# Optimization experiments

Measured on AMD Instinct MI355X. Metric: run time of the kernel, lower is better.

The kernel has to match this reference:

```python
import jax, jax.numpy as jnp
import numpy as np

B, H, KVH, D = 32, 32, 8, 128          # batch, q heads, kv heads, head_size
S = 2048                                # context length per sequence
BLOCK_SIZE = 16                         # tokens per cache block
NUM_BLOCKS = B * (S // BLOCK_SIZE)      # 4096
BASE = 10000.0
SCALE = 1.0 / D ** 0.5


def setup_inputs() -> dict:
    key = jax.random.key(0)
    kq, kk, kv = jax.random.split(key, 3)
    query = jax.random.normal(kq, (B, H, D), dtype=jnp.float32)
    # paged KV cache: [num_blocks, block_size * kv_heads * head_size]
    k_cache = jax.random.normal(kk, (NUM_BLOCKS, BLOCK_SIZE * KVH * D), dtype=jnp.float32)
    v_cache = jax.random.normal(kv, (NUM_BLOCKS, BLOCK_SIZE * KVH * D), dtype=jnp.float32)
    # contiguous slot layout: slot[i, p] = i * S + p  (>=0 means valid)
    slot_mapping = jnp.arange(B * S, dtype=jnp.int32).reshape(B, S)
    # per-sequence token positions 0..S-1
    positions = jnp.broadcast_to(jnp.arange(S, dtype=jnp.int32), (B, S))
    return {"query": query, "k_cache": k_cache, "v_cache": v_cache,
            "slot_mapping": slot_mapping, "positions": positions}


def _rope(x, pos):
    """x: [B, h, s, D], pos: [B, s] int -> rotary-embedded x (RotaryEmbedding.forward)."""
    inv_freq = 1.0 / (BASE ** (jnp.arange(0, D, 2, dtype=jnp.float32) / D))   # [D/2]
    freqs = pos[..., None].astype(jnp.float32) * inv_freq                     # [B, s, D/2]
    emb = jnp.concatenate([freqs, freqs], axis=-1)                            # [B, s, D]
    cos = jnp.cos(emb)[:, None]                                               # [B, 1, s, D]
    sin = jnp.sin(emb)[:, None]
    x1, x2 = x[..., : D // 2], x[..., D // 2 :]
    rotated = jnp.concatenate([-x2, x1], axis=-1)
    return x * cos + rotated * sin


def reference(query, k_cache, v_cache, slot_mapping, positions):
    # --- paged gather (the per-slot loop in _compatible_forward, vectorized) ---
    valid = slot_mapping >= 0                                  # [B, S]
    slots = jnp.where(valid, slot_mapping, 0)
    blk = slots // BLOCK_SIZE
    off = slots % BLOCK_SIZE
    kc = k_cache.reshape(NUM_BLOCKS, BLOCK_SIZE, KVH, D)
    vc = v_cache.reshape(NUM_BLOCKS, BLOCK_SIZE, KVH, D)
    k = kc[blk, off]                                           # [B, S, KVH, D]
    v = vc[blk, off]
    m = valid[..., None, None]
    k = jnp.where(m, k, 0.0).transpose(0, 2, 1, 3)             # [B, KVH, S, D]
    v = jnp.where(m, v, 0.0).transpose(0, 2, 1, 3)

    # --- rotary: q at its (last) position, keys at all cached positions ---
    q = query[:, :, None, :]                                   # [B, H, 1, D]
    q = _rope(q, positions[:, -1:])
    k = _rope(k, positions)

    # --- GQA: repeat_interleave kv heads to match q heads ---
    rep = H // KVH
    k = jnp.repeat(k, rep, axis=1)                             # [B, H, S, D]
    v = jnp.repeat(v, rep, axis=1)

    scores = jnp.einsum('bhqd,bhkd->bhqk', q, k) * SCALE       # [B, H, 1, S]
    weights = jax.nn.softmax(scores, axis=-1)
    out = jnp.einsum('bhqk,bhkd->bhqd', weights, v)            # [B, H, 1, D]
    return out[:, :, 0, :]                                     # [B, H, D]
```

## Files before the change

kernel.cpp:

```cpp
#include <hip/hip_runtime.h>
#include <math.h>

#define B_    32
#define H_    32
#define KVH_  8
#define D_    128
#define S_    2048
#define REP   4
#define PAIRS 256
#define SCALE 0.08838834764831845f


__global__ __launch_bounds__(256) void pa_main(
    const float* __restrict__ query,
    const float* __restrict__ k_cache,
    const float* __restrict__ v_cache,
    const int*   __restrict__ slot_map,
    const int*   __restrict__ positions,
    float* __restrict__ ws_l,
    float* __restrict__ ws_acc,
    float* __restrict__ out,
    int nsplit)
{
    const int pair  = blockIdx.x / nsplit;
    const int split = blockIdx.x % nsplit;
    const int b     = pair >> 3;
    const int kvh   = pair & 7;
    const int tid   = threadIdx.x;
    const int lane  = tid & 63;
    const int wave  = tid >> 6;
    const int g     = lane & 15;
    const int ts    = lane >> 4;

    float invf[4];
    #pragma unroll
    for (int j = 0; j < 4; j++)
        invf[j] = (float)exp(-(double)(4*g + j) * (9.210340371976184 / 64.0));

    const int posq = positions[b * S_ + (S_ - 1)];
    float ql[4][4], qh[4][4];
    #pragma unroll
    for (int hh = 0; hh < REP; hh++) {
        const float4* qb = (const float4*)(query + (size_t)(b * H_ + kvh * REP + hh) * D_);
        float4 a = qb[g];
        float4 c = qb[16 + g];
        float al[4] = {a.x, a.y, a.z, a.w};
        float ah[4] = {c.x, c.y, c.z, c.w};
        #pragma unroll
        for (int j = 0; j < 4; j++) {
            double fr = (double)posq * exp(-(double)(4*g + j) * (9.210340371976184 / 64.0));
            float cs = (float)cos(fr), sn = (float)sin(fr);
            ql[hh][j] = (al[j] * cs - ah[j] * sn) * SCALE;
            qh[hh][j] = (ah[j] * cs + al[j] * sn) * SCALE;
        }
    }

    const int chunk  = S_ / nsplit;
    const int wtok   = chunk >> 2;
    const int passes = wtok >> 2;
    const int t0     = split * chunk + wave * wtok;
    const int bS     = b * S_;

    float acc_lo[4][4] = {};
    float acc_hi[4][4] = {};
    float lsum[4] = {0.f, 0.f, 0.f, 0.f};

    int slot = slot_map[bS + t0 + ts];
    int pos  = positions[bS + t0 + ts];
    int sc   = slot < 0 ? 0 : slot;
    const float4* kb = (const float4*)(k_cache + (size_t)(sc >> 4) * 16384 + (size_t)(sc & 15) * 1024 + kvh * 128);
    const float4* vb = (const float4*)(v_cache + (size_t)(sc >> 4) * 16384 + (size_t)(sc & 15) * 1024 + kvh * 128);
    float4 k1 = kb[g], k2 = kb[16 + g], v1 = vb[g], v2 = vb[16 + g];

    for (int i = 0; i < passes; i++) {
        int nslot = 0, npos = 0;
        float4 nk1 = {0,0,0,0}, nk2 = {0,0,0,0}, nv1 = {0,0,0,0}, nv2 = {0,0,0,0};
        const bool more = (i + 1 < passes);
        if (more) {
            const int st = t0 + (i + 1) * 4 + ts;
            nslot = slot_map[bS + st];
            npos  = positions[bS + st];
            const int nsc = nslot < 0 ? 0 : nslot;
            const float4* nkb = (const float4*)(k_cache + (size_t)(nsc >> 4) * 16384 + (size_t)(nsc & 15) * 1024 + kvh * 128);
            const float4* nvb = (const float4*)(v_cache + (size_t)(nsc >> 4) * 16384 + (size_t)(nsc & 15) * 1024 + kvh * 128);
            nk1 = nkb[g]; nk2 = nkb[16 + g]; nv1 = nvb[g]; nv2 = nvb[16 + g];
        }

        const float m  = (slot >= 0) ? 1.f : 0.f;
        const float pf = (float)pos;
        float kx[4] = {k1.x, k1.y, k1.z, k1.w};
        float ky[4] = {k2.x, k2.y, k2.z, k2.w};
        float vx[4] = {v1.x * m, v1.y * m, v1.z * m, v1.w * m};
        float vy[4] = {v2.x * m, v2.y * m, v2.z * m, v2.w * m};
        float kl[4], kh[4];
        #pragma unroll
        for (int j = 0; j < 4; j++) {
            float fr = pf * invf[j];
            float sn, cs;
            __sincosf(fr, &sn, &cs);
            kl[j] = (kx[j] * cs - ky[j] * sn) * m;
            kh[j] = (ky[j] * cs + kx[j] * sn) * m;
        }

        float p[4];
        #pragma unroll
        for (int hh = 0; hh < 4; hh++) {
            float t = ql[hh][0] * kl[0];
            t += ql[hh][1] * kl[1];
            t += ql[hh][2] * kl[2];
            t += ql[hh][3] * kl[3];
            t += qh[hh][0] * kh[0];
            t += qh[hh][1] * kh[1];
            t += qh[hh][2] * kh[2];
            t += qh[hh][3] * kh[3];
            p[hh] = t;
        }
        #pragma unroll
        for (int hh = 0; hh < 4; hh++) {
            #pragma unroll
            for (int mm = 1; mm < 16; mm <<= 1)
                p[hh] += __shfl_xor(p[hh], mm);
        }
        #pragma unroll
        for (int hh = 0; hh < 4; hh++) {
            const float w = __expf(p[hh]);
            lsum[hh] += w;
            #pragma unroll
            for (int j = 0; j < 4; j++) {
                acc_lo[hh][j] += w * vx[j];
                acc_hi[hh][j] += w * vy[j];
            }
        }

        slot = nslot; pos = npos;
        k1 = nk1; k2 = nk2; v1 = nv1; v2 = nv2;
    }

    #pragma unroll
    for (int hh = 0; hh < 4; hh++) {
        lsum[hh] += __shfl_xor(lsum[hh], 16);
        lsum[hh] += __shfl_xor(lsum[hh], 32);
        #pragma unroll
        for (int j = 0; j < 4; j++) {
            acc_lo[hh][j] += __shfl_xor(acc_lo[hh][j], 16);
            acc_lo[hh][j] += __shfl_xor(acc_lo[hh][j], 32);
            acc_hi[hh][j] += __shfl_xor(acc_hi[hh][j], 16);
            acc_hi[hh][j] += __shfl_xor(acc_hi[hh][j], 32);
        }
    }

    __shared__ float lds_acc[4][4][128];
    __shared__ float lds_l[4][4];
    if (lane < 16) {
        #pragma unroll
        for (int hh = 0; hh < 4; hh++)
            #pragma unroll
            for (int j = 0; j < 4; j++) {
                lds_acc[wave][hh][4*g + j]      = acc_lo[hh][j];
                lds_acc[wave][hh][64 + 4*g + j] = acc_hi[hh][j];
            }
    }
    if (lane == 0) {
        #pragma unroll
        for (int hh = 0; hh < 4; hh++) lds_l[wave][hh] = lsum[hh];
    }
    __syncthreads();

    for (int v = tid; v < 512; v += 256) {
        const int hh = v >> 7, d = v & 127;
        const float a = lds_acc[0][hh][d] + lds_acc[1][hh][d] + lds_acc[2][hh][d] + lds_acc[3][hh][d];
        if (nsplit > 1) {
            ws_acc[((size_t)(pair * nsplit + split) * 4 + hh) * 128 + d] = a;
        } else {
            const float lt = lds_l[0][hh] + lds_l[1][hh] + lds_l[2][hh] + lds_l[3][hh];
            out[((size_t)(b * H_ + kvh * REP + hh)) * D_ + d] = a / lt;
        }
    }
    if (nsplit > 1 && tid < 4) {
        ws_l[(pair * nsplit + split) * 4 + tid] =
            lds_l[0][tid] + lds_l[1][tid] + lds_l[2][tid] + lds_l[3][tid];
    }
}

__global__ __launch_bounds__(512) void pa_reduce(
    const float* __restrict__ ws_l,
    const float* __restrict__ ws_acc,
    float* __restrict__ out,
    int nsplit)
{
    const int pair = blockIdx.x;
    const int b = pair >> 3, kvh = pair & 7;
    const int hh = threadIdx.x >> 7;
    const int d  = threadIdx.x & 127;
    float a = 0.f;
    for (int s = 0; s < nsplit; s++)
        a += ws_acc[((size_t)(pair * nsplit + s) * 4 + hh) * 128 + d];
    float lt = 0.f;
    for (int s = 0; s < nsplit; s++)
        lt += ws_l[(pair * nsplit + s) * 4 + hh];
    out[((size_t)(b * H_ + kvh * REP + hh)) * D_ + d] = a / lt;
}

extern "C" void kernel_launch(void* const* d_in, const int* in_sizes, int n_in,
                              void* d_out, int out_size, void* d_ws, size_t ws_size,
                              hipStream_t stream) {
    const float* query = (const float*)d_in[0];
    const float* kc    = (const float*)d_in[1];
    const float* vc    = (const float*)d_in[2];
    const int*   sm    = (const int*)d_in[3];
    const int*   pos   = (const int*)d_in[4];
    float* out = (float*)d_out;

    int nsplit = 1;
    const int cands[3] = {8, 4, 2};
    for (int c = 0; c < 3; c++) {
        size_t need = (size_t)PAIRS * cands[c] * (4 + 512) * sizeof(float);
        if (ws_size >= need) { nsplit = cands[c]; break; }
    }

    float* ws_l   = (float*)d_ws;
    float* ws_acc = ws_l + (size_t)PAIRS * nsplit * 4;

    pa_main<<<dim3(PAIRS * nsplit), dim3(256), 0, stream>>>(
        query, kc, vc, sm, pos, ws_l, ws_acc, out, nsplit);
    if (nsplit > 1)
        pa_reduce<<<dim3(PAIRS), dim3(512), 0, stream>>>(ws_l, ws_acc, out, nsplit);
}
```

Measured before the change: 548.4 us.

## Stream KV via async global-to-LDS loads with per-wave splits and precomputed q rope

Moves the KV gather onto double-buffered async global_load_lds copies, tracked with vmcnt waits. Each wave now owns its own sequence chunk, with up to 32 splits per pair, so the block-level LDS reduction and __syncthreads go away. A small pre-kernel applies rope to q once and builds the inverse-frequency table, which removes the double-precision trig from every main block. Slot and position indices are staged in LDS. The aim is more memory parallelism and less per-block setup, at the cost of an extra launch and a larger reduce workspace.

```diff
diff --git a/kernel.cpp b/kernel.cpp
--- a/kernel.cpp
+++ b/kernel.cpp
@@ -10,96 +10,156 @@
 #define PAIRS 256
 #define SCALE 0.08838834764831845f
 
-
-__global__ __launch_bounds__(256) void pa_main(
+typedef unsigned int u32;
+
+__device__ __forceinline__ void dma16(const float* g, float* l) {
+    __builtin_amdgcn_global_load_lds(
+        (const __attribute__((address_space(1))) u32*)g,
+        (__attribute__((address_space(3))) u32*)l,
+        16, 0, 0);
+}
+
+#define WAITVM(N) asm volatile("s_waitcnt vmcnt(" #N ")" ::: "memory")
+
+__global__ __launch_bounds__(64) void rope_q(
+    const float* __restrict__ query,
+    const int*   __restrict__ positions,
+    float* __restrict__ q_rot,
+    float* __restrict__ invf_tab)
+{
+    const int head = blockIdx.x;
+    const int b    = head >> 5;
+    const int j    = threadIdx.x;
+    const double invf = exp(-(double)j * (9.210340371976184 / 64.0));
+    if (head == 0) invf_tab[j] = (float)invf;
+    const int posq = positions[b * S_ + (S_ - 1)];
+    const double fr = (double)posq * invf;
+    const float cs = (float)cos(fr), sn = (float)sin(fr);
+    const float* q = query + (size_t)head * D_;
+    const float lo = q[j], hi = q[64 + j];
+    float* o = q_rot + (size_t)head * D_;
+    o[j]      = (lo * cs - hi * sn) * SCALE;
+    o[64 + j] = (hi * cs + lo * sn) * SCALE;
+}
+
+extern __shared__ char smem_raw[];
+
+__global__ __launch_bounds__(128, 4) void pa_main(
     const float* __restrict__ query,
     const float* __restrict__ k_cache,
     const float* __restrict__ v_cache,
     const int*   __restrict__ slot_map,
     const int*   __restrict__ positions,
+    const float* __restrict__ q_rot,
+    const float* __restrict__ invf_tab,
     float* __restrict__ ws_l,
     float* __restrict__ ws_acc,
     float* __restrict__ out,
-    int nsplit)
+    int cpp, int wpb, int use_qrot)
 {
-    const int pair  = blockIdx.x / nsplit;
-    const int split = blockIdx.x % nsplit;
+    const int w     = threadIdx.x >> 6;
+    const int ln    = threadIdx.x & 63;
+    const int g     = ln & 15;
+    const int ts    = ln >> 4;
+    const int chunk = S_ / cpp;
+    const int gch   = blockIdx.x * wpb + w;
+    const int pair  = gch / cpp;
+    const int c     = gch - pair * cpp;
     const int b     = pair >> 3;
     const int kvh   = pair & 7;
-    const int tid   = threadIdx.x;
-    const int lane  = tid & 63;
-    const int wave  = tid >> 6;
-    const int g     = lane & 15;
-    const int ts    = lane >> 4;
-
-    float invf[4];
-    #pragma unroll
-    for (int j = 0; j < 4; j++)
-        invf[j] = (float)exp(-(double)(4*g + j) * (9.210340371976184 / 64.0));
-
-    const int posq = positions[b * S_ + (S_ - 1)];
-    float ql[4][4], qh[4][4];
-    #pragma unroll
-    for (int hh = 0; hh < REP; hh++) {
-        const float4* qb = (const float4*)(query + (size_t)(b * H_ + kvh * REP + hh) * D_);
-        float4 a = qb[g];
-        float4 c = qb[16 + g];
-        float al[4] = {a.x, a.y, a.z, a.w};
-        float ah[4] = {c.x, c.y, c.z, c.w};
-        #pragma unroll
-        for (int j = 0; j < 4; j++) {
-            double fr = (double)posq * exp(-(double)(4*g + j) * (9.210340371976184 / 64.0));
-            float cs = (float)cos(fr), sn = (float)sin(fr);
-            ql[hh][j] = (al[j] * cs - ah[j] * sn) * SCALE;
-            qh[hh][j] = (ah[j] * cs + al[j] * sn) * SCALE;
-        }
-    }
-
-    const int chunk  = S_ / nsplit;
-    const int wtok   = chunk >> 2;
-    const int passes = wtok >> 2;
-    const int t0     = split * chunk + wave * wtok;
-    const int bS     = b * S_;
+    const int t0    = c * chunk;
+    const int bS    = b * S_;
+    const int passes = chunk >> 2;
+
+    char*  wbase = smem_raw + (size_t)w * (8192 + 8 * chunk);
+    float* buf   = (float*)wbase;
+    int*   ls    = (int*)(wbase + 8192);
+    int*   lp    = ls + chunk;
+
+    for (int t = ln; t < chunk; t += 64) {
+        ls[t] = slot_map[bS + t0 + t];
+        lp[t] = positions[bS + t0 + t];
+    }
+
+    float ql[4][4], qh[4][4], invf[4];
+    if (use_qrot) {
+        float4 iv = ((const float4*)invf_tab)[g];
+        invf[0] = iv.x; invf[1] = iv.y; invf[2] = iv.z; invf[3] = iv.w;
+        #pragma unroll
+        for (int hh = 0; hh < REP; hh++) {
+            const float4* qb = (const float4*)(q_rot + (size_t)(b * H_ + kvh * REP + hh) * D_);
+            float4 a = qb[g], cc = qb[16 + g];
+            ql[hh][0] = a.x;  ql[hh][1] = a.y;  ql[hh][2] = a.z;  ql[hh][3] = a.w;
+            qh[hh][0] = cc.x; qh[hh][1] = cc.y; qh[hh][2] = cc.z; qh[hh][3] = cc.w;
+        }
+    } else {
+        #pragma unroll
+        for (int j = 0; j < 4; j++)
+            invf[j] = (float)exp(-(double)(4 * g + j) * (9.210340371976184 / 64.0));
+        const int posq = positions[bS + (S_ - 1)];
+        #pragma unroll
+        for (int hh = 0; hh < REP; hh++) {
+            const float4* qb = (const float4*)(query + (size_t)(b * H_ + kvh * REP + hh) * D_);
+            float4 a = qb[g], cc = qb[16 + g];
+            float al[4] = {a.x, a.y, a.z, a.w};
+            float ah[4] = {cc.x, cc.y, cc.z, cc.w};
+            #pragma unroll
+            for (int j = 0; j < 4; j++) {
+                double fr = (double)posq * exp(-(double)(4 * g + j) * (9.210340371976184 / 64.0));
+                float cs = (float)cos(fr), sn = (float)sin(fr);
+                ql[hh][j] = (al[j] * cs - ah[j] * sn) * SCALE;
+                qh[hh][j] = (ah[j] * cs + al[j] * sn) * SCALE;
+            }
+        }
+    }
 
     float acc_lo[4][4] = {};
     float acc_hi[4][4] = {};
     float lsum[4] = {0.f, 0.f, 0.f, 0.f};
 
-    int slot = slot_map[bS + t0 + ts];
-    int pos  = positions[bS + t0 + ts];
-    int sc   = slot < 0 ? 0 : slot;
-    const float4* kb = (const float4*)(k_cache + (size_t)(sc >> 4) * 16384 + (size_t)(sc & 15) * 1024 + kvh * 128);
-    const float4* vb = (const float4*)(v_cache + (size_t)(sc >> 4) * 16384 + (size_t)(sc & 15) * 1024 + kvh * 128);
-    float4 k1 = kb[g], k2 = kb[16 + g], v1 = vb[g], v2 = vb[16 + g];
-
-    for (int i = 0; i < passes; i++) {
-        int nslot = 0, npos = 0;
-        float4 nk1 = {0,0,0,0}, nk2 = {0,0,0,0}, nv1 = {0,0,0,0}, nv2 = {0,0,0,0};
-        const bool more = (i + 1 < passes);
-        if (more) {
-            const int st = t0 + (i + 1) * 4 + ts;
-            nslot = slot_map[bS + st];
-            npos  = positions[bS + st];
-            const int nsc = nslot < 0 ? 0 : nslot;
-            const float4* nkb = (const float4*)(k_cache + (size_t)(nsc >> 4) * 16384 + (size_t)(nsc & 15) * 1024 + kvh * 128);
-            const float4* nvb = (const float4*)(v_cache + (size_t)(nsc >> 4) * 16384 + (size_t)(nsc & 15) * 1024 + kvh * 128);
-            nk1 = nkb[g]; nk2 = nkb[16 + g]; nv1 = nvb[g]; nv2 = nvb[16 + g];
-        }
-
-        const float m  = (slot >= 0) ? 1.f : 0.f;
-        const float pf = (float)pos;
-        float kx[4] = {k1.x, k1.y, k1.z, k1.w};
-        float ky[4] = {k2.x, k2.y, k2.z, k2.w};
-        float vx[4] = {v1.x * m, v1.y * m, v1.z * m, v1.w * m};
-        float vy[4] = {v2.x * m, v2.y * m, v2.z * m, v2.w * m};
+    auto issue = [&](int pi, int bi) {
+        const int tix = pi * 4 + ts;
+        const int sl  = ls[tix];
+        const int sc  = sl < 0 ? 0 : sl;
+        const int ro  = (sc >> 4) * 16384 + (sc & 15) * 1024 + kvh * 128 + 4 * g;
+        const float* kr = k_cache + ro;
+        const float* vr = v_cache + ro;
+        float* bp = buf + bi * 1024;
+        dma16(kr,      bp);
+        dma16(kr + 64, bp + 256);
+        dma16(vr,      bp + 512);
+        dma16(vr + 64, bp + 768);
+    };
+
+    issue(0, 0);
+    for (int i = 0; i < passes; ++i) {
+        const int ni = (i + 1 < passes) ? i + 1 : i;
+        issue(ni, (i + 1) & 1);
+
+        WAITVM(4);
+        __builtin_amdgcn_sched_barrier(0);
+
+        const float4* bf4 = (const float4*)(buf + (i & 1) * 1024);
+        float4 k1 = bf4[ln];
+        float4 k2 = bf4[64 + ln];
+
+        const int tix = i * 4 + ts;
+        const int sl  = ls[tix];
+        const float m  = (sl >= 0) ? 1.f : 0.f;
+        const float pf = (float)lp[tix];
+
         float kl[4], kh[4];
-        #pragma unroll
-        for (int j = 0; j < 4; j++) {
-            float fr = pf * invf[j];
-            float sn, cs;
-            __sincosf(fr, &sn, &cs);
-            kl[j] = (kx[j] * cs - ky[j] * sn) * m;
-            kh[j] = (ky[j] * cs + kx[j] * sn) * m;
+        {
+            float kx[4] = {k1.x, k1.y, k1.z, k1.w};
+            float ky[4] = {k2.x, k2.y, k2.z, k2.w};
+            #pragma unroll
+            for (int j = 0; j < 4; j++) {
+                float fr = pf * invf[j];
+                float sn, cs;
+                __sincosf(fr, &sn, &cs);
+                kl[j] = (kx[j] * cs - ky[j] * sn) * m;
+                kh[j] = (ky[j] * cs + kx[j] * sn) * m;
+            }
         }
 
         float p[4];
@@ -121,20 +181,24 @@
             for (int mm = 1; mm < 16; mm <<= 1)
                 p[hh] += __shfl_xor(p[hh], mm);
         }
+
+        float4 v1 = bf4[128 + ln];
+        float4 v2 = bf4[192 + ln];
+        float vx[4] = {v1.x * m, v1.y * m, v1.z * m, v1.w * m};
+        float vy[4] = {v2.x * m, v2.y * m, v2.z * m, v2.w * m};
+
         #pragma unroll
         for (int hh = 0; hh < 4; hh++) {
-            const float w = __expf(p[hh]);
-            lsum[hh] += w;
+            const float wgt = __expf(p[hh]);
+            lsum[hh] += wgt;
             #pragma unroll
             for (int j = 0; j < 4; j++) {
-                acc_lo[hh][j] += w * vx[j];
-                acc_hi[hh][j] += w * vy[j];
-            }
-        }
-
-        slot = nslot; pos = npos;
-        k1 = nk1; k2 = nk2; v1 = nv1; v2 = nv2;
-    }
+                acc_lo[hh][j] += wgt * vx[j];
+                acc_hi[hh][j] += wgt * vy[j];
+            }
+        }
+    }
+    WAITVM(0);
 
     #pragma unroll
     for (int hh = 0; hh < 4; hh++) {
@@ -149,36 +213,28 @@
         }
     }
 
-    __shared__ float lds_acc[4][4][128];
-    __shared__ float lds_l[4][4];
-    if (lane < 16) {
-        #pragma unroll
-        for (int hh = 0; hh < 4; hh++)
-            #pragma unroll
-            for (int j = 0; j < 4; j++) {
-                lds_acc[wave][hh][4*g + j]      = acc_lo[hh][j];
-                lds_acc[wave][hh][64 + 4*g + j] = acc_hi[hh][j];
-            }
-    }
-    if (lane == 0) {
-        #pragma unroll
-        for (int hh = 0; hh < 4; hh++) lds_l[wave][hh] = lsum[hh];
-    }
-    __syncthreads();
-
-    for (int v = tid; v < 512; v += 256) {
-        const int hh = v >> 7, d = v & 127;
-        const float a = lds_acc[0][hh][d] + lds_acc[1][hh][d] + lds_acc[2][hh][d] + lds_acc[3][hh][d];
-        if (nsplit > 1) {
-            ws_acc[((size_t)(pair * nsplit + split) * 4 + hh) * 128 + d] = a;
-        } else {
-            const float lt = lds_l[0][hh] + lds_l[1][hh] + lds_l[2][hh] + lds_l[3][hh];
-            out[((size_t)(b * H_ + kvh * REP + hh)) * D_ + d] = a / lt;
-        }
-    }
-    if (nsplit > 1 && tid < 4) {
-        ws_l[(pair * nsplit + split) * 4 + tid] =
-            lds_l[0][tid] + lds_l[1][tid] + lds_l[2][tid] + lds_l[3][tid];
+    if (cpp > 1) {
+        if (ln < 16) {
+            const size_t base = (size_t)(pair * cpp + c) * 4;
+            #pragma unroll
+            for (int hh = 0; hh < 4; hh++) {
+                float4* dst = (float4*)(ws_acc + (base + hh) * 128);
+                dst[g]      = make_float4(acc_lo[hh][0], acc_lo[hh][1], acc_lo[hh][2], acc_lo[hh][3]);
+                dst[16 + g] = make_float4(acc_hi[hh][0], acc_hi[hh][1], acc_hi[hh][2], acc_hi[hh][3]);
+            }
+            if (ln == 0)
+                *(float4*)(ws_l + base) = make_float4(lsum[0], lsum[1], lsum[2], lsum[3]);
+        }
+    } else {
+        if (ln < 16) {
+            #pragma unroll
+            for (int hh = 0; hh < 4; hh++) {
+                const float r = 1.f / lsum[hh];
+                float4* dst = (float4*)(out + (size_t)(b * H_ + kvh * REP + hh) * D_);
+                dst[g]      = make_float4(acc_lo[hh][0] * r, acc_lo[hh][1] * r, acc_lo[hh][2] * r, acc_lo[hh][3] * r);
+                dst[16 + g] = make_float4(acc_hi[hh][0] * r, acc_hi[hh][1] * r, acc_hi[hh][2] * r, acc_hi[hh][3] * r);
+            }
+        }
     }
 }
 
@@ -186,18 +242,18 @@
     const float* __restrict__ ws_l,
     const float* __restrict__ ws_acc,
     float* __restrict__ out,
-    int nsplit)
+    int cpp)
 {
     const int pair = blockIdx.x;
     const int b = pair >> 3, kvh = pair & 7;
     const int hh = threadIdx.x >> 7;
     const int d  = threadIdx.x & 127;
     float a = 0.f;
-    for (int s = 0; s < nsplit; s++)
-        a += ws_acc[((size_t)(pair * nsplit + s) * 4 + hh) * 128 + d];
+    for (int s = 0; s < cpp; s++)
+        a += ws_acc[((size_t)(pair * cpp + s) * 4 + hh) * 128 + d];
     float lt = 0.f;
-    for (int s = 0; s < nsplit; s++)
-        lt += ws_l[(pair * nsplit + s) * 4 + hh];
+    for (int s = 0; s < cpp; s++)
+        lt += ws_l[(pair * cpp + s) * 4 + hh];
     out[((size_t)(b * H_ + kvh * REP + hh)) * D_ + d] = a / lt;
 }
 
@@ -211,18 +267,29 @@
     const int*   pos   = (const int*)d_in[4];
     float* out = (float*)d_out;
 
-    int nsplit = 1;
-    const int cands[3] = {8, 4, 2};
-    for (int c = 0; c < 3; c++) {
-        size_t need = (size_t)PAIRS * cands[c] * (4 + 512) * sizeof(float);
-        if (ws_size >= need) { nsplit = cands[c]; break; }
-    }
-
-    float* ws_l   = (float*)d_ws;
-    float* ws_acc = ws_l + (size_t)PAIRS * nsplit * 4;
-
-    pa_main<<<dim3(PAIRS * nsplit), dim3(256), 0, stream>>>(
-        query, kc, vc, sm, pos, ws_l, ws_acc, out, nsplit);
-    if (nsplit > 1)
-        pa_reduce<<<dim3(PAIRS), dim3(512), 0, stream>>>(ws_l, ws_acc, out, nsplit);
-}
+    const size_t qrot_f = (size_t)B_ * H_ * D_ + 64;
+    int cpp = 1;
+    int use_qrot = 0;
+    const int cands[5] = {32, 16, 8, 4, 2};
+    for (int ci = 0; ci < 5; ci++) {
+        size_t need = (qrot_f + (size_t)PAIRS * cands[ci] * 516) * sizeof(float);
+        if (ws_size >= need) { cpp = cands[ci]; use_qrot = 1; break; }
+    }
+    if (cpp == 1 && ws_size >= qrot_f * sizeof(float)) use_qrot = 1;
+
+    float* q_rot    = (float*)d_ws;
+    float* invf_tab = q_rot + (size_t)B_ * H_ * D_;
+    float* ws_l     = use_qrot ? (invf_tab + 64) : (float*)d_ws;
+    float* ws_acc   = ws_l + (size_t)PAIRS * cpp * 4;
+
+    if (use_qrot)
+        rope_q<<<dim3(B_ * H_), dim3(64), 0, stream>>>(query, pos, q_rot, invf_tab);
+
+    const int wpb   = (cpp >= 2) ? 2 : 1;
+    const int chunk = S_ / cpp;
+    const size_t dynlds = (size_t)wpb * (8192 + 8 * chunk);
+    pa_main<<<dim3(PAIRS * cpp / wpb), dim3(64 * wpb), dynlds, stream>>>(
+        query, kc, vc, sm, pos, q_rot, invf_tab, ws_l, ws_acc, out, cpp, wpb, use_qrot);
+    if (cpp > 1)
+        pa_reduce<<<dim3(PAIRS), dim3(512), 0, stream>>>(ws_l, ws_acc, out, cpp);
+}
```

Result: no change. 552.8 us (+0.8%).
